# Kernel tuning notes

Hardware: AMD Instinct MI355X
Metric: run time of the kernel (lower is better)

The kernel has to match this reference:

```python
import jax, jax.numpy as jnp
import numpy as np

N_NODES = 100_000
N_EDGES = 6_400_000
CH = 5


def setup_inputs() -> dict:
    key = jax.random.key(0)
    ks = jax.random.split(key, 16)
    inp = {
        "x": jax.random.normal(ks[0], (N_NODES, 2), dtype=jnp.float32),
        "edge_index": jax.random.randint(ks[1], (2, N_EDGES), 0, N_NODES, dtype=jnp.int64 if jax.config.jax_enable_x64 else jnp.int32).astype(jnp.int32),
        "edge_attr": jax.random.uniform(ks[2], (N_EDGES, 1), dtype=jnp.float32),
        "lin1_w": jax.random.normal(ks[3], (2, CH), dtype=jnp.float32) * 0.5,
        "lin1_b": jax.random.normal(ks[4], (CH,), dtype=jnp.float32) * 0.1,
        "conv1_wf": jax.random.normal(ks[5], (2 * CH + 1, CH), dtype=jnp.float32) * 0.3,
        "conv1_bf": jax.random.normal(ks[6], (CH,), dtype=jnp.float32) * 0.1,
        "conv1_ws": jax.random.normal(ks[7], (2 * CH + 1, CH), dtype=jnp.float32) * 0.3,
        "conv1_bs": jax.random.normal(ks[8], (CH,), dtype=jnp.float32) * 0.1,
        "conv2_wf": jax.random.normal(ks[9], (2 * CH + 1, CH), dtype=jnp.float32) * 0.3,
        "conv2_bf": jax.random.normal(ks[10], (CH,), dtype=jnp.float32) * 0.1,
        "conv2_ws": jax.random.normal(ks[11], (2 * CH + 1, CH), dtype=jnp.float32) * 0.3,
        "conv2_bs": jax.random.normal(ks[12], (CH,), dtype=jnp.float32) * 0.1,
        "lin2_w": jax.random.normal(ks[13], (CH, 2), dtype=jnp.float32) * 0.5,
        "lin2_b": jax.random.normal(ks[14], (2,), dtype=jnp.float32) * 0.1,
    }
    return inp


def cgconv(x, edge_index, edge_attr, wf, bf, ws, bs):
    # PyG CGConv: x_i' = x_i + sum_{j->i} sigmoid(z W_f + b_f) * softplus(z W_s + b_s)
    # z = [x_i, x_j, e_ij]; edge_index[0]=source j, edge_index[1]=target i
    src, dst = edge_index[0], edge_index[1]
    z = jnp.concatenate([x[dst], x[src], edge_attr], axis=-1)  # [E, 2C+dim]
    msg = jax.nn.sigmoid(z @ wf + bf) * jax.nn.softplus(z @ ws + bs)  # [E, C]
    agg = jax.ops.segment_sum(msg, dst, num_segments=x.shape[0])  # [N, C]
    return x + agg


def reference(x, edge_index, edge_attr,
              lin1_w, lin1_b,
              conv1_wf, conv1_bf, conv1_ws, conv1_bs,
              conv2_wf, conv2_bf, conv2_ws, conv2_bs,
              lin2_w, lin2_b):
    h = x @ lin1_w + lin1_b  # [N, C]
    h = cgconv(h, edge_index, edge_attr, conv1_wf, conv1_bf, conv1_ws, conv1_bs)
    h = cgconv(h, edge_index, edge_attr, conv2_wf, conv2_bf, conv2_ws, conv2_bs)
    return h @ lin2_w + lin2_b  # [N, 2]
```

## Files before the change

kernel.cpp:

```cpp
#include <hip/hip_runtime.h>
#include <hip/hip_fp16.h>

constexpr int NN = 100000;
constexpr int NE = 6400000;
constexpr int BSH = 7;
constexpr int BN = 1 << BSH;
constexpr int NBUCK = (NN + BN - 1) / BN;
constexpr int BCAP = 9216;
constexpr int STILE = 8192;
constexpr int NSB = (NE + STILE - 1) / STILE;
constexpr int NP = 1024;
constexpr int GS = 16;

#define LOG2E 1.44269504f
#define LN2   0.69314718f


__global__ __launch_bounds__(256) void k_lin2(const float* __restrict__ h,
                                              const float* __restrict__ w,
                                              const float* __restrict__ b,
                                              float* __restrict__ out) {
    int n = blockIdx.x * 256 + threadIdx.x;
    if (n >= NN) return;
    float o0 = b[0], o1 = b[1];
#pragma unroll
    for (int c = 0; c < 5; ++c) {
        float hv = h[(size_t)n * 5 + c];
        o0 += hv * w[2 * c];
        o1 += hv * w[2 * c + 1];
    }
    out[2 * n] = o0;
    out[2 * n + 1] = o1;
}

__device__ __forceinline__ void prep_core(const float hv[5],
                                          const float* __restrict__ wf,
                                          const float* __restrict__ bf,
                                          const float* __restrict__ ws,
                                          const float* __restrict__ bs,
                                          int n, float* __restrict__ TD,
                                          unsigned short* __restrict__ TSh) {
    float tg[5], ts[5], sg[5], ss[5];
#pragma unroll
    for (int c = 0; c < 5; ++c) {
        float a = bf[c], d = bs[c], u = 0.f, v = 0.f;
#pragma unroll
        for (int k = 0; k < 5; ++k) {
            a += hv[k] * wf[k * 5 + c];
            d += hv[k] * ws[k * 5 + c];
            u += hv[k] * wf[(5 + k) * 5 + c];
            v += hv[k] * ws[(5 + k) * 5 + c];
        }
        tg[c] = -a * LOG2E; ts[c] = -d * LOG2E;
        sg[c] = -u * LOG2E; ss[c] = -v * LOG2E;
    }
    float4* Dp = (float4*)(TD + (size_t)n * 12);
    Dp[0] = make_float4(tg[0], tg[1], tg[2], tg[3]);
    Dp[1] = make_float4(tg[4], ts[0], ts[1], ts[2]);
    Dp[2] = make_float4(ts[3], ts[4], 0.f, 0.f);

    unsigned p[5];
#pragma unroll
    for (int c = 0; c < 5; ++c) {
        unsigned lo = (unsigned)__half_as_ushort(__float2half_rn(sg[c]));
        unsigned hi = (unsigned)__half_as_ushort(__float2half_rn(ss[c]));
        p[c] = lo | (hi << 16);
    }
    uint4 w0 = make_uint4(p[0], p[1], p[2], p[3]);
    uint4 w1 = make_uint4(p[4], 0u, 0u, 0u);
    *(uint4*)(TSh + (size_t)n * 16) = w0;
    *(uint4*)(TSh + (size_t)n * 16 + 8) = w1;
}

__global__ __launch_bounds__(256) void k_prep1(const float* __restrict__ x,
                                               const float* __restrict__ l1w,
                                               const float* __restrict__ l1b,
                                               const float* __restrict__ wf,
                                               const float* __restrict__ bf,
                                               const float* __restrict__ ws,
                                               const float* __restrict__ bs,
                                               float* __restrict__ TD,
                                               unsigned short* __restrict__ TSh,
                                               float* __restrict__ h) {
    int n = blockIdx.x * 256 + threadIdx.x;
    if (n >= NN) return;
    float x0 = x[2 * n], x1 = x[2 * n + 1];
    float hv[5];
#pragma unroll
    for (int c = 0; c < 5; ++c) {
        hv[c] = l1b[c] + x0 * l1w[c] + x1 * l1w[5 + c];
        h[(size_t)n * 5 + c] = hv[c];
    }
    prep_core(hv, wf, bf, ws, bs, n, TD, TSh);
}

__global__ __launch_bounds__(256) void k_prep(const float* __restrict__ h,
                                              const float* __restrict__ wf,
                                              const float* __restrict__ bf,
                                              const float* __restrict__ ws,
                                              const float* __restrict__ bs,
                                              float* __restrict__ TD,
                                              unsigned short* __restrict__ TSh) {
    int n = blockIdx.x * 256 + threadIdx.x;
    if (n >= NN) return;
    float hv[5];
#pragma unroll
    for (int k = 0; k < 5; ++k) hv[k] = h[(size_t)n * 5 + k];
    prep_core(hv, wf, bf, ws, bs, n, TD, TSh);
}

__global__ __launch_bounds__(256) void k_initcurs(int* __restrict__ gcurs) {
    int i = blockIdx.x * 256 + threadIdx.x;
    if (i < NBUCK) gcurs[(size_t)i * GS] = i * BCAP;
}

__global__ __launch_bounds__(512) void k_scatter4(const int* __restrict__ ei,
                                                  const float* __restrict__ ea,
                                                  int* __restrict__ gcurs,
                                                  unsigned int* __restrict__ rec) {
    __shared__ unsigned int lrec[STILE];
    __shared__ unsigned int spk[STILE];
    __shared__ int C[NBUCK];
    __shared__ int loc[NBUCK];
    __shared__ int gbase[NBUCK];
    __shared__ int A[NP];
    const int tid = threadIdx.x, blk = blockIdx.x;
    const int base = blk * STILE;
    const int m = min(STILE, NE - base);

    for (int i = tid; i < NBUCK; i += 512) C[i] = 0;
    __syncthreads();

    const int m4 = m >> 2;
    const int4* s4 = (const int4*)(ei + base);
    const int4* d4 = (const int4*)(ei + NE + base);
    const float4* a4 = (const float4*)(ea + base);
    for (int q = tid; q < m4; q += 512) {
        int4 s = s4[q];
        int4 d = d4[q];
        float4 a = a4[q];
        int k = q * 4;
        lrec[k + 0] = (unsigned)s.x | ((unsigned)(d.x & (BN - 1)) << 17) |
                      (__float2uint_rn(a.x * 255.f) << 24);
        lrec[k + 1] = (unsigned)s.y | ((unsigned)(d.y & (BN - 1)) << 17) |
                      (__float2uint_rn(a.y * 255.f) << 24);
        lrec[k + 2] = (unsigned)s.z | ((unsigned)(d.z & (BN - 1)) << 17) |
                      (__float2uint_rn(a.z * 255.f) << 24);
        lrec[k + 3] = (unsigned)s.w | ((unsigned)(d.w & (BN - 1)) << 17) |
                      (__float2uint_rn(a.w * 255.f) << 24);
        atomicAdd(&C[(unsigned)d.x >> BSH], 1);
        atomicAdd(&C[(unsigned)d.y >> BSH], 1);
        atomicAdd(&C[(unsigned)d.z >> BSH], 1);
        atomicAdd(&C[(unsigned)d.w >> BSH], 1);
    }
    __syncthreads();

    for (int b = tid; b < NBUCK; b += 512)
        gbase[b] = C[b] ? atomicAdd(&gcurs[(size_t)b * GS], C[b]) : 0;
    for (int i = tid; i < NP; i += 512) A[i] = (i < NBUCK) ? C[i] : 0;
    __syncthreads();

    for (int d = 1; d < NP; d <<= 1) {
        int i = (tid + 1) * (d << 1) - 1;
        if (i < NP) A[i] += A[i - d];
        __syncthreads();
    }
    if (tid == 0) A[NP - 1] = 0;
    __syncthreads();
    for (int d = NP >> 1; d >= 1; d >>= 1) {
        int i = (tid + 1) * (d << 1) - 1;
        if (i < NP) { int t = A[i - d]; A[i - d] = A[i]; A[i] += t; }
        __syncthreads();
    }
    for (int b = tid; b < NBUCK; b += 512) loc[b] = A[b];
    __syncthreads();

    for (int k = tid; k < m; k += 512) {
        int bkt = (unsigned)ei[NE + base + k] >> BSH;
        int p = atomicAdd(&loc[bkt], 1);
        spk[p] = (unsigned)k | ((unsigned)bkt << 16);
    }
    __syncthreads();

    for (int p = tid; p < m; p += 512) {
        unsigned pk = spk[p];
        int k = pk & 0xFFFF;
        int bkt = pk >> 16;
        rec[gbase[bkt] + (p - A[bkt])] = lrec[k];
    }
}

__global__ __launch_bounds__(512) void k_sortbkt(const int* __restrict__ gcurs,
                                                 unsigned int* __restrict__ rec,
                                                 int2* __restrict__ nrange) {
    __shared__ unsigned int lrec[BCAP];
    __shared__ int cnt[BN];
    __shared__ int curs[BN];
    const int b = blockIdx.x, tid = threadIdx.x;
    const int e0 = b * BCAP;
    const int m = gcurs[(size_t)b * GS] - e0;
    const int node0 = b << BSH;
    const int nloc = min(BN, NN - node0);

    for (int i = tid; i < m; i += 512) lrec[i] = rec[e0 + i];
    if (tid < BN) cnt[tid] = 0;
    __syncthreads();
    for (int i = tid; i < m; i += 512)
        atomicAdd(&cnt[(lrec[i] >> 17) & (BN - 1)], 1);
    __syncthreads();
    int v = (tid < BN) ? cnt[tid] : 0;
    for (int off = 1; off < BN; off <<= 1) {
        int t = 0;
        if (tid < BN && tid >= off) t = cnt[tid - off];
        __syncthreads();
        if (tid < BN) cnt[tid] += t;
        __syncthreads();
    }
    if (tid < BN) {
        int excl = cnt[tid] - v;
        curs[tid] = excl;
        if (tid < nloc)
            nrange[node0 + tid] = make_int2(e0 + excl, e0 + excl + v);
    }
    __syncthreads();
    for (int i = tid; i < m; i += 512) {
        unsigned int r = lrec[i];
        int dl = (r >> 17) & (BN - 1);
        int pos = atomicAdd(&curs[dl], 1);
        rec[e0 + pos] = r;
    }
}

__global__ __launch_bounds__(256) void k_conv_csr(
        const unsigned int* __restrict__ rec, const int2* __restrict__ nrange,
        const float* __restrict__ TD, const unsigned short* __restrict__ TSh,
        const float* __restrict__ wf, const float* __restrict__ ws,
        float* __restrict__ h ) {
    const int tid = threadIdx.x;
    const int lane = tid & 15;
    const int n = blockIdx.x * 16 + (tid >> 4);

    __half2 we2[5];
#pragma unroll
    for (int c = 0; c < 5; ++c)
        we2[c] = __floats2half2_rn(-wf[50 + c] * LOG2E, -ws[50 + c] * LOG2E);

    const float4* Dp = (const float4*)(TD + (size_t)n * 12);
    float4 d0 = Dp[0], d1 = Dp[1], d2 = Dp[2];
    const float Tg[5] = {d0.x, d0.y, d0.z, d0.w, d1.x};
    const float Ts[5] = {d1.y, d1.z, d1.w, d2.x, d2.y};
    __half2 dd2[5];
#pragma unroll
    for (int c = 0; c < 5; ++c) dd2[c] = __floats2half2_rn(Tg[c], Ts[c]);

    const __half2 one2 = __float2half2_rn(1.f);
    const __half hz = __float2half(0.f);

    float acc[5] = {0.f, 0.f, 0.f, 0.f, 0.f};
    const int2 rg = nrange[n];
    const int eEnd = rg.y;
    for (int e = rg.x + lane; e < eEnd; e += 64) {
        unsigned r[4];
        bool vld[4];
        float4 q0[4];
        unsigned q1[4];
        __half2 a2[4];
#pragma unroll
        for (int j = 0; j < 4; ++j) {
            int ej = e + j * 16;
            vld[j] = ej < eEnd;
            r[j] = rec[vld[j] ? ej : e];
        }
#pragma unroll
        for (int j = 0; j < 4; ++j) {
            const unsigned src = r[j] & 0x1FFFFu;
            const unsigned short* row = TSh + (size_t)src * 16;
            q0[j] = *(const float4*)row;
            q1[j] = *(const unsigned*)(row + 8);
            a2[j] = __float2half2_rn((float)(r[j] >> 24) * (1.f / 255.f));
        }
#pragma unroll
        for (int j = 0; j < 4; ++j) {
            if (!vld[j]) continue;
            union { float4 f; __half2 h2[4]; } u; u.f = q0[j];
            __half2 s2[5] = {u.h2[0], u.h2[1], u.h2[2], u.h2[3],
                             *(__half2*)&q1[j]};
#pragma unroll
            for (int c = 0; c < 5; ++c) {
                __half2 z2 = __hadd2(__hfma2(a2[j], we2[c], dd2[c]), s2[c]);
                __half zx = __low2half(z2);
                __half zy = __high2half(z2);
                __half nab = __hmin(zy, __hneg(zy));
                __half2 e2 = h2exp2(__halves2half2(zx, nab));
                __half2 o2 = __hadd2(e2, one2);
                float sig = __half2float(hrcp(__low2half(o2)));
                float lg  = __half2float(hlog2(__high2half(o2)));
                float mx  = __half2float(__hmin(zy, hz));
                acc[c] = fmaf(sig, lg - mx, acc[c]);
            }
        }
    }
#pragma unroll
    for (int off = 8; off >= 1; off >>= 1)
#pragma unroll
        for (int c = 0; c < 5; ++c)
            acc[c] += __shfl_xor(acc[c], off, 16);
    if (lane == 0) {
#pragma unroll
        for (int c = 0; c < 5; ++c)
            h[(size_t)n * 5 + c] += LN2 * acc[c];
    }
}

__global__ __launch_bounds__(256) void k_prep_fb(const float* __restrict__ h,
                                                 const float* __restrict__ wf,
                                                 const float* __restrict__ bf,
                                                 const float* __restrict__ ws,
                                                 const float* __restrict__ bs,
                                                 float* __restrict__ T,
                                                 float* __restrict__ S,
                                                 float* __restrict__ hout) {
    int n = blockIdx.x * 256 + threadIdx.x;
    if (n >= NN) return;
    float hv[5];
#pragma unroll
    for (int k = 0; k < 5; ++k) hv[k] = h[5 * n + k];
    float tf[5], ts[5], sf[5], ss[5];
#pragma unroll
    for (int c = 0; c < 5; ++c) {
        float a = bf[c], d = bs[c], u = 0.f, v = 0.f;
#pragma unroll
        for (int k = 0; k < 5; ++k) {
            a += hv[k] * wf[k * 5 + c];
            d += hv[k] * ws[k * 5 + c];
            u += hv[k] * wf[(5 + k) * 5 + c];
            v += hv[k] * ws[(5 + k) * 5 + c];
        }
        tf[c] = a; ts[c] = d; sf[c] = u; ss[c] = v;
    }
    float4* Tp = (float4*)(T + (size_t)n * 16);
    Tp[0] = make_float4(tf[0], tf[1], tf[2], tf[3]);
    Tp[1] = make_float4(tf[4], ts[0], ts[1], ts[2]);
    Tp[2] = make_float4(ts[3], ts[4], 0.f, 0.f);
    float4* Sp = (float4*)(S + (size_t)n * 16);
    Sp[0] = make_float4(sf[0], sf[1], sf[2], sf[3]);
    Sp[1] = make_float4(sf[4], ss[0], ss[1], ss[2]);
    Sp[2] = make_float4(ss[3], ss[4], 0.f, 0.f);
#pragma unroll
    for (int c = 0; c < 5; ++c) hout[5 * n + c] = hv[c];
}

__global__ __launch_bounds__(256) void k_conv_atomic(const int* __restrict__ ei,
                                                     const float* __restrict__ ea,
                                                     const float* __restrict__ T,
                                                     const float* __restrict__ S,
                                                     const float* __restrict__ wf,
                                                     const float* __restrict__ ws,
                                                     float* __restrict__ hout) {
    int e = blockIdx.x * 256 + threadIdx.x;
    if (e >= NE) return;
    int src = ei[e];
    int dst = ei[NE + e];
    float a = ea[e];
    const float4* Tp = (const float4*)(T + (size_t)dst * 16);
    const float4* Sp = (const float4*)(S + (size_t)src * 16);
    float4 t0 = Tp[0], t1 = Tp[1], t2 = Tp[2];
    float4 s0 = Sp[0], s1 = Sp[1], s2 = Sp[2];
    float za[5] = {t0.x + s0.x, t0.y + s0.y, t0.z + s0.z, t0.w + s0.w, t1.x + s1.x};
    float zs[5] = {t1.y + s1.y, t1.z + s1.z, t1.w + s1.w, t2.x + s2.x, t2.y + s2.y};
    float* outp = hout + (size_t)dst * 5;
#pragma unroll
    for (int c = 0; c < 5; ++c) {
        float f = za[c] + a * wf[50 + c];
        float s = zs[c] + a * ws[50 + c];
        float sig = 1.f / (1.f + __expf(-f));
        float sp = __logf(1.f + __expf(-fabsf(s))) + fmaxf(s, 0.f);
        unsafeAtomicAdd(outp + c, sig * sp);
    }
}

__global__ __launch_bounds__(256) void k_lin1_fb(const float* __restrict__ x,
                                                 const float* __restrict__ w,
                                                 const float* __restrict__ b,
                                                 float* __restrict__ h) {
    int n = blockIdx.x * 256 + threadIdx.x;
    if (n >= NN) return;
    float x0 = x[2 * n], x1 = x[2 * n + 1];
#pragma unroll
    for (int c = 0; c < 5; ++c)
        h[5 * n + c] = b[c] + x0 * w[c] + x1 * w[5 + c];
}

extern "C" void kernel_launch(void* const* d_in, const int* in_sizes, int n_in,
                              void* d_out, int out_size, void* d_ws, size_t ws_size,
                              hipStream_t stream) {
    const float* x    = (const float*)d_in[0];
    const int*   ei   = (const int*)d_in[1];
    const float* ea   = (const float*)d_in[2];
    const float* l1w  = (const float*)d_in[3];
    const float* l1b  = (const float*)d_in[4];
    const float* c1wf = (const float*)d_in[5];
    const float* c1bf = (const float*)d_in[6];
    const float* c1ws = (const float*)d_in[7];
    const float* c1bs = (const float*)d_in[8];
    const float* c2wf = (const float*)d_in[9];
    const float* c2bf = (const float*)d_in[10];
    const float* c2ws = (const float*)d_in[11];
    const float* c2bs = (const float*)d_in[12];
    const float* l2w  = (const float*)d_in[13];
    const float* l2b  = (const float*)d_in[14];
    float* out = (float*)d_out;
    char* ws = (char*)d_ws;

    size_t o_rec    = 0;
    size_t o_nrange = o_rec + (size_t)NBUCK * BCAP * 4;
    size_t o_gcurs  = o_nrange + (size_t)NN * 8;
    size_t o_TD     = (o_gcurs + (size_t)NBUCK * GS * 4 + 15) & ~(size_t)15;
    size_t o_TS     = o_TD + (size_t)NN * 12 * 4;
    size_t o_h      = o_TS + (size_t)NN * 16 * 2;
    size_t need     = o_h + (size_t)NN * 5 * 4;

    int nb_n = (NN + 255) / 256;

    if (ws_size >= need) {
        unsigned int* rec    = (unsigned int*)(ws + o_rec);
        int2* nrange         = (int2*)(ws + o_nrange);
        int* gcurs           = (int*)(ws + o_gcurs);
        float* TD            = (float*)(ws + o_TD);
        unsigned short* TSh  = (unsigned short*)(ws + o_TS);
        float* h             = (float*)(ws + o_h);

        k_initcurs<<<(NBUCK + 255) / 256, 256, 0, stream>>>(gcurs);
        k_scatter4<<<NSB,   512, 0, stream>>>(ei, ea, gcurs, rec);
        k_sortbkt <<<NBUCK, 512, 0, stream>>>(gcurs, rec, nrange);

        k_prep1<<<nb_n, 256, 0, stream>>>(x, l1w, l1b,
                                          c1wf, c1bf, c1ws, c1bs, TD, TSh, h);
        k_conv_csr<<<NN / 16, 256, 0, stream>>>(rec, nrange, TD, TSh,
                                                c1wf, c1ws, h);
        k_prep<<<nb_n, 256, 0, stream>>>(h, c2wf, c2bf, c2ws, c2bs, TD, TSh);
        k_conv_csr<<<NN / 16, 256, 0, stream>>>(rec, nrange, TD, TSh,
                                                c2wf, c2ws, h);
        k_lin2<<<nb_n, 256, 0, stream>>>(h, l2w, l2b, out);
    } else {
        float* h0 = (float*)(ws);
        float* h1 = (float*)(ws + 2000000);
        float* h2 = h0;
        float* T  = (float*)(ws + 4000000);
        float* S  = (float*)(ws + 10400000);
        int nb_e = (NE + 255) / 256;

        k_lin1_fb<<<nb_n, 256, 0, stream>>>(x, l1w, l1b, h0);
        k_prep_fb<<<nb_n, 256, 0, stream>>>(h0, c1wf, c1bf, c1ws, c1bs, T, S, h1);
        k_conv_atomic<<<nb_e, 256, 0, stream>>>(ei, ea, T, S, c1wf, c1ws, h1);
        k_prep_fb<<<nb_n, 256, 0, stream>>>(h1, c2wf, c2bf, c2ws, c2bs, T, S, h2);
        k_conv_atomic<<<nb_e, 256, 0, stream>>>(ei, ea, T, S, c2wf, c2ws, h2);
        k_lin2<<<nb_n, 256, 0, stream>>>(h2, l2w, l2b, out);
    }
}
```

Baseline: 210.3 us.

## Halve scatter tile, use wave-shuffle bucket scan, cache bucket ids in LDS

The edge-scatter kernel now takes 4096-edge tiles instead of 8192. Its Blelloch shared-memory scan, which needed about 20 barriers, becomes a two-level wavefront shuffle scan with only a few barriers. Destination bucket ids are cached in LDS as 16-bit values, so the second pass no longer re-reads the edge index from global memory, and the sort keys shrink to 16 bits. The global bucket cursors are packed densely instead of padded to 16 ints apart, which raises contention on shared cache lines, and doubling the block count doubles the global cursor atomics.

```diff
diff --git a/kernel.cpp b/kernel.cpp
--- a/kernel.cpp
+++ b/kernel.cpp
@@ -7,10 +7,9 @@
 constexpr int BN = 1 << BSH;
 constexpr int NBUCK = (NN + BN - 1) / BN;
 constexpr int BCAP = 9216;
-constexpr int STILE = 8192;
+constexpr int STILE = 4096;
 constexpr int NSB = (NE + STILE - 1) / STILE;
 constexpr int NP = 1024;
-constexpr int GS = 16;
 
 #define LOG2E 1.44269504f
 #define LN2   0.69314718f
@@ -111,19 +110,21 @@
 
 __global__ __launch_bounds__(256) void k_initcurs(int* __restrict__ gcurs) {
     int i = blockIdx.x * 256 + threadIdx.x;
-    if (i < NBUCK) gcurs[(size_t)i * GS] = i * BCAP;
-}
-
-__global__ __launch_bounds__(512) void k_scatter4(const int* __restrict__ ei,
+    if (i < NBUCK) gcurs[i] = i * BCAP;
+}
+
+__global__ __launch_bounds__(512) void k_scatter5(const int* __restrict__ ei,
                                                   const float* __restrict__ ea,
                                                   int* __restrict__ gcurs,
                                                   unsigned int* __restrict__ rec) {
     __shared__ unsigned int lrec[STILE];
-    __shared__ unsigned int spk[STILE];
+    __shared__ unsigned short lbkt[STILE];
+    __shared__ unsigned short spk[STILE];
     __shared__ int C[NBUCK];
     __shared__ int loc[NBUCK];
     __shared__ int gbase[NBUCK];
     __shared__ int A[NP];
+    __shared__ int wsum[16];
     const int tid = threadIdx.x, blk = blockIdx.x;
     const int base = blk * STILE;
     const int m = min(STILE, NE - base);
@@ -148,6 +149,10 @@
                       (__float2uint_rn(a.z * 255.f) << 24);
         lrec[k + 3] = (unsigned)s.w | ((unsigned)(d.w & (BN - 1)) << 17) |
                       (__float2uint_rn(a.w * 255.f) << 24);
+        lbkt[k + 0] = (unsigned short)((unsigned)d.x >> BSH);
+        lbkt[k + 1] = (unsigned short)((unsigned)d.y >> BSH);
+        lbkt[k + 2] = (unsigned short)((unsigned)d.z >> BSH);
+        lbkt[k + 3] = (unsigned short)((unsigned)d.w >> BSH);
         atomicAdd(&C[(unsigned)d.x >> BSH], 1);
         atomicAdd(&C[(unsigned)d.y >> BSH], 1);
         atomicAdd(&C[(unsigned)d.z >> BSH], 1);
@@ -156,36 +161,57 @@
     __syncthreads();
 
     for (int b = tid; b < NBUCK; b += 512)
-        gbase[b] = C[b] ? atomicAdd(&gcurs[(size_t)b * GS], C[b]) : 0;
-    for (int i = tid; i < NP; i += 512) A[i] = (i < NBUCK) ? C[i] : 0;
-    __syncthreads();
-
-    for (int d = 1; d < NP; d <<= 1) {
-        int i = (tid + 1) * (d << 1) - 1;
-        if (i < NP) A[i] += A[i - d];
-        __syncthreads();
-    }
-    if (tid == 0) A[NP - 1] = 0;
-    __syncthreads();
-    for (int d = NP >> 1; d >= 1; d >>= 1) {
-        int i = (tid + 1) * (d << 1) - 1;
-        if (i < NP) { int t = A[i - d]; A[i - d] = A[i]; A[i] += t; }
-        __syncthreads();
-    }
-    for (int b = tid; b < NBUCK; b += 512) loc[b] = A[b];
+        gbase[b] = C[b] ? atomicAdd(&gcurs[b], C[b]) : 0;
+
+    const int lane = tid & 63;
+    const int wv = tid >> 6;
+    int orig[2], incl[2];
+#pragma unroll
+    for (int half = 0; half < 2; ++half) {
+        int c = wv + half * 8;
+        int i = c * 64 + lane;
+        int v = (i < NBUCK) ? C[i] : 0;
+        orig[half] = v;
+#pragma unroll
+        for (int off = 1; off < 64; off <<= 1) {
+            int t = __shfl_up(v, off, 64);
+            if (lane >= off) v += t;
+        }
+        incl[half] = v;
+        if (lane == 63) wsum[c] = v;
+    }
+    __syncthreads();
+    if (tid < 16) {
+        int v = wsum[tid];
+#pragma unroll
+        for (int off = 1; off < 16; off <<= 1) {
+            int t = __shfl_up(v, off, 16);
+            if (tid >= off) v += t;
+        }
+        wsum[tid] = v;
+    }
+    __syncthreads();
+#pragma unroll
+    for (int half = 0; half < 2; ++half) {
+        int c = wv + half * 8;
+        int i = c * 64 + lane;
+        int coff = (c > 0) ? wsum[c - 1] : 0;
+        int excl = incl[half] - orig[half] + coff;
+        A[i] = excl;
+        if (i < NBUCK) loc[i] = excl;
+    }
     __syncthreads();
 
     for (int k = tid; k < m; k += 512) {
-        int bkt = (unsigned)ei[NE + base + k] >> BSH;
+        int bkt = lbkt[k];
         int p = atomicAdd(&loc[bkt], 1);
-        spk[p] = (unsigned)k | ((unsigned)bkt << 16);
+        spk[p] = (unsigned short)k;
     }
     __syncthreads();
 
     for (int p = tid; p < m; p += 512) {
-        unsigned pk = spk[p];
-        int k = pk & 0xFFFF;
-        int bkt = pk >> 16;
+        int k = spk[p];
+        int bkt = lbkt[k];
         rec[gbase[bkt] + (p - A[bkt])] = lrec[k];
     }
 }
@@ -198,7 +224,7 @@
     __shared__ int curs[BN];
     const int b = blockIdx.x, tid = threadIdx.x;
     const int e0 = b * BCAP;
-    const int m = gcurs[(size_t)b * GS] - e0;
+    const int m = gcurs[b] - e0;
     const int node0 = b << BSH;
     const int nloc = min(BN, NN - node0);
 
@@ -415,7 +441,7 @@
     size_t o_rec    = 0;
     size_t o_nrange = o_rec + (size_t)NBUCK * BCAP * 4;
     size_t o_gcurs  = o_nrange + (size_t)NN * 8;
-    size_t o_TD     = (o_gcurs + (size_t)NBUCK * GS * 4 + 15) & ~(size_t)15;
+    size_t o_TD     = (o_gcurs + (size_t)NBUCK * 4 + 15) & ~(size_t)15;
     size_t o_TS     = o_TD + (size_t)NN * 12 * 4;
     size_t o_h      = o_TS + (size_t)NN * 16 * 2;
     size_t need     = o_h + (size_t)NN * 5 * 4;
@@ -431,7 +457,7 @@
         float* h             = (float*)(ws + o_h);
 
         k_initcurs<<<(NBUCK + 255) / 256, 256, 0, stream>>>(gcurs);
-        k_scatter4<<<NSB,   512, 0, stream>>>(ei, ea, gcurs, rec);
+        k_scatter5<<<NSB,   512, 0, stream>>>(ei, ea, gcurs, rec);
         k_sortbkt <<<NBUCK, 512, 0, stream>>>(gcurs, rec, nrange);
 
         k_prep1<<<nb_n, 256, 0, stream>>>(x, l1w, l1b,
```

New measurement: 200.0 us. 4.9% less time.
